# Kernel optimization log

Measured on AMD Instinct MI355X. Metric: run time of the kernel, lower is better.

Reference implementation:

```python
import jax, jax.numpy as jnp
import numpy as np
from jax import lax

DN = ('NCH', 'OIH', 'NCH')

def conv1d(x, w, b, pad=0):
    y = lax.conv_general_dilated(x, w, window_strides=(1,), padding=[(pad, pad)], dimension_numbers=DN)
    return y + b[None, :, None]

def conv_transpose1d(x, w_torch, b):
    # torch ConvTranspose1d weight: [C_in, C_out, K]; equivalent to full conv with flipped kernel
    k = w_torch.shape[-1]
    w = jnp.flip(jnp.transpose(w_torch, (1, 0, 2)), axis=-1)  # [C_out, C_in, K]
    y = lax.conv_general_dilated(x, w, window_strides=(1,), padding=[(k - 1, k - 1)], dimension_numbers=DN)
    return y + b[None, :, None]

def converter(signal, w1, b1, w2, b2, wt, bt, w3, b3):
    h = jax.nn.relu(conv1d(signal, w1, b1))          # [B,10,n-2]
    h = jax.nn.relu(conv1d(h, w2, b2))               # [B,10,n-2]
    h = jax.nn.relu(conv_transpose1d(h, wt, bt))     # [B,10,n]
    h = jax.nn.sigmoid(conv1d(h, w3, b3))            # [B,2,n]
    return h

def setup_inputs() -> dict:
    key = jax.random.key(0)
    ks = jax.random.split(key, 12)
    B, C, n = 32, 128, 8192
    signal = jax.random.normal(ks[0], (B, C, n), dtype=jnp.float32)
    curr_diag = jax.random.uniform(ks[1], (B, n - 1), dtype=jnp.float32) + 0.5
    s = 0.1
    return {
        'signal': signal,
        'curr_diag': curr_diag,
        'index_diag': 1,
        'w1': jax.random.normal(ks[2], (10, C, 3), dtype=jnp.float32) * s,
        'b1': jax.random.normal(ks[3], (10,), dtype=jnp.float32) * s,
        'w2': jax.random.normal(ks[4], (10, 10, 1), dtype=jnp.float32) * s,
        'b2': jax.random.normal(ks[5], (10,), dtype=jnp.float32) * s,
        'wt': jax.random.normal(ks[6], (10, 10, 3), dtype=jnp.float32) * s,
        'bt': jax.random.normal(ks[7], (10,), dtype=jnp.float32) * s,
        'w3': jax.random.normal(ks[8], (2, 10, 1), dtype=jnp.float32) * s,
        'b3': jax.random.normal(ks[9], (2,), dtype=jnp.float32) * s,
        'const': jnp.float32(0.99),
    }

def reference(signal, curr_diag, index_diag, w1, b1, w2, b2, wt, bt, w3, b3, const):
    n = signal.shape[-1]
    lr = converter(signal, w1, b1, w2, b2, wt, bt, w3, b3)  # [B,2,n]
    left, right = lr[:, 0, :], lr[:, 1, :]
    # diag_len = n - index_diag; next diag has length diag_len - 1
    mass_in = curr_diag[:, 1:] * right[:, 1:n - index_diag]
    mass_in = mass_in + curr_diag[:, :-1] * left[:, index_diag:n - 1]
    mass_out = right[:, 0:n - index_diag - 1] + left[:, index_diag + 1:n]
    next_diag = const * mass_in / mass_out
    next_diag = jnp.log(next_diag)
    next_diag = next_diag - jnp.mean(next_diag)
    return next_diag
```

## Files before the change

### kernel.cpp

```cpp
#include <hip/hip_runtime.h>
#include <math.h>

#define B   32
#define CIN 128
#define NN  8192
#define N1  8190
#define CH  10

__global__ __launch_bounds__(256) void k1_conv12(
    const float* __restrict__ sig, const float* __restrict__ w1, const float* __restrict__ b1,
    const float* __restrict__ w2, const float* __restrict__ b2, float* __restrict__ h2out)
{
    const int t = blockIdx.x * 256 + threadIdx.x;
    const int b = blockIdx.y;
    if (t >= N1) return;

    float acc[CH];
#pragma unroll
    for (int o = 0; o < CH; ++o) acc[o] = b1[o];

    const float* sp = sig + (size_t)b * CIN * NN + t;
    for (int ci = 0; ci < CIN; ++ci) {
        const float s0 = sp[(size_t)ci * NN + 0];
        const float s1 = sp[(size_t)ci * NN + 1];
        const float s2 = sp[(size_t)ci * NN + 2];
        const float* wp = w1 + ci * 3;
#pragma unroll
        for (int o = 0; o < CH; ++o) {
            acc[o] = fmaf(wp[o * CIN * 3 + 0], s0, acc[o]);
            acc[o] = fmaf(wp[o * CIN * 3 + 1], s1, acc[o]);
            acc[o] = fmaf(wp[o * CIN * 3 + 2], s2, acc[o]);
        }
    }

    float h1[CH];
#pragma unroll
    for (int o = 0; o < CH; ++o) h1[o] = fmaxf(acc[o], 0.f);

#pragma unroll
    for (int o = 0; o < CH; ++o) {
        float a = b2[o];
#pragma unroll
        for (int i = 0; i < CH; ++i) a = fmaf(w2[o * CH + i], h1[i], a);
        h2out[((size_t)b * CH + o) * N1 + t] = fmaxf(a, 0.f);
    }
}

__global__ __launch_bounds__(256) void k2_convt3(
    const float* __restrict__ h2, const float* __restrict__ wt, const float* __restrict__ bt,
    const float* __restrict__ w3, const float* __restrict__ b3, float* __restrict__ lr)
{
    const int t = blockIdx.x * 256 + threadIdx.x;
    const int b = blockIdx.y;
    if (t >= NN) return;

    float acc[CH];
#pragma unroll
    for (int o = 0; o < CH; ++o) acc[o] = bt[o];

#pragma unroll
    for (int i = 0; i < CH; ++i) {
        const float* hp = h2 + ((size_t)b * CH + i) * N1;
        const float v0 = (t < N1)               ? hp[t]     : 0.f;
        const float v1 = (t >= 1 && t <= N1)    ? hp[t - 1] : 0.f;
        const float v2 = (t >= 2)               ? hp[t - 2] : 0.f;
        const float* wp = wt + (i * CH) * 3;
#pragma unroll
        for (int o = 0; o < CH; ++o) {
            acc[o] = fmaf(wp[o * 3 + 0], v0, acc[o]);
            acc[o] = fmaf(wp[o * 3 + 1], v1, acc[o]);
            acc[o] = fmaf(wp[o * 3 + 2], v2, acc[o]);
        }
    }

    float l = b3[0], r = b3[1];
#pragma unroll
    for (int o = 0; o < CH; ++o) {
        const float h3 = fmaxf(acc[o], 0.f);
        l = fmaf(w3[o],      h3, l);
        r = fmaf(w3[CH + o], h3, r);
    }
    l = 1.f / (1.f + expf(-l));
    r = 1.f / (1.f + expf(-r));

    lr[((size_t)b * 2 + 0) * NN + t] = l;
    lr[((size_t)b * 2 + 1) * NN + t] = r;
}

__global__ __launch_bounds__(256) void k3_diag(
    const float* __restrict__ lr, const float* __restrict__ cd,
    const float* __restrict__ cstp, float* __restrict__ outv, float* __restrict__ bsums)
{
    const int t = blockIdx.x * 256 + threadIdx.x;
    const int b = blockIdx.y;
    float v = 0.f;
    if (t < N1) {
        const float c0 = cd[(size_t)b * (NN - 1) + t];
        const float c1 = cd[(size_t)b * (NN - 1) + t + 1];
        const float* lp = lr + (size_t)b * 2 * NN;
        const float* rp = lp + NN;
        const float mi = c1 * rp[t + 1] + c0 * lp[t + 1];
        const float mo = rp[t] + lp[t + 2];
        v = logf(cstp[0] * mi / mo);
        outv[(size_t)b * N1 + t] = v;
    }
    __shared__ float red[256];
    red[threadIdx.x] = v;
    __syncthreads();
#pragma unroll
    for (int s = 128; s > 0; s >>= 1) {
        if (threadIdx.x < s) red[threadIdx.x] += red[threadIdx.x + s];
        __syncthreads();
    }
    if (threadIdx.x == 0) bsums[blockIdx.y * gridDim.x + blockIdx.x] = red[0];
}

__global__ __launch_bounds__(256) void k4_mean(const float* __restrict__ bsums, float* __restrict__ meanp)
{
    __shared__ float red[256];
    float s = 0.f;
    for (int i = threadIdx.x; i < 1024; i += 256) s += bsums[i];
    red[threadIdx.x] = s;
    __syncthreads();
#pragma unroll
    for (int st = 128; st > 0; st >>= 1) {
        if (threadIdx.x < st) red[threadIdx.x] += red[threadIdx.x + st];
        __syncthreads();
    }
    if (threadIdx.x == 0) meanp[0] = red[0] / (float)(B * N1);
}

__global__ __launch_bounds__(256) void k5_sub(float* __restrict__ outv, const float* __restrict__ meanp, int n)
{
    const int i = blockIdx.x * 256 + threadIdx.x;
    if (i < n) outv[i] -= meanp[0];
}

extern "C" void kernel_launch(void* const* d_in, const int* in_sizes, int n_in,
                              void* d_out, int out_size, void* d_ws, size_t ws_size,
                              hipStream_t stream)
{
    const float* sig = (const float*)d_in[0];
    const float* cd  = (const float*)d_in[1];
    const float* w1  = (const float*)d_in[3];
    const float* b1  = (const float*)d_in[4];
    const float* w2  = (const float*)d_in[5];
    const float* b2  = (const float*)d_in[6];
    const float* wt  = (const float*)d_in[7];
    const float* bt  = (const float*)d_in[8];
    const float* w3  = (const float*)d_in[9];
    const float* b3  = (const float*)d_in[10];
    const float* cst = (const float*)d_in[11];

    float* outv = (float*)d_out;

    float* ws   = (float*)d_ws;
    float* h2   = ws;
    float* lr   = h2 + (size_t)B * CH * N1;
    float* bsum = lr + (size_t)B * 2 * NN;
    float* mean = bsum + 1024;

    dim3 blk(256);
    dim3 g1((N1 + 255) / 256, B);
    dim3 g2(NN / 256, B);

    k1_conv12<<<g1, blk, 0, stream>>>(sig, w1, b1, w2, b2, h2);
    k2_convt3<<<g2, blk, 0, stream>>>(h2, wt, bt, w3, b3, lr);
    k3_diag  <<<g1, blk, 0, stream>>>(lr, cd, cst, outv, bsum);
    k4_mean  <<<dim3(1), blk, 0, stream>>>(bsum, mean);
    k5_sub   <<<dim3((out_size + 255) / 256), blk, 0, stream>>>(outv, mean, out_size);
}
```

Before: 258.5 us.

## Fuse transposed conv with diag kernel and compute two outputs per thread in conv1

The first conv kernel now has each thread compute two adjacent time positions, using float2 loads so the three-tap window overlaps between them and weight loads are shared. The transposed-conv/sigmoid kernel is fused with the diagonal/log kernel, keeping the left/right gates in shared memory with a small halo instead of round-tripping through global memory. This drops one launch and the lr buffer traffic. The cost is a few redundant halo positions per tile, computed by a second pass of the loop, and halving conv1's thread count, which lowers occupancy on a memory-bound kernel.

```diff
diff --git a/kernel.cpp b/kernel.cpp
--- a/kernel.cpp
+++ b/kernel.cpp
@@ -1,109 +1,120 @@
 #include <hip/hip_runtime.h>
 #include <math.h>
 
-#define B   32
-#define CIN 128
-#define NN  8192
-#define N1  8190
-#define CH  10
+#define B    32
+#define CIN  128
+#define NN   8192
+#define N1   8190
+#define CH   10
+#define TILE 256
 
 __global__ __launch_bounds__(256) void k1_conv12(
     const float* __restrict__ sig, const float* __restrict__ w1, const float* __restrict__ b1,
     const float* __restrict__ w2, const float* __restrict__ b2, float* __restrict__ h2out)
 {
-    const int t = blockIdx.x * 256 + threadIdx.x;
-    const int b = blockIdx.y;
-    if (t >= N1) return;
+    const int p  = blockIdx.x * 256 + threadIdx.x;
+    const int t2 = 2 * p;
+    const int b  = blockIdx.y;
+    if (t2 >= N1) return;
 
-    float acc[CH];
+    float y0[CH], y1[CH];
 #pragma unroll
-    for (int o = 0; o < CH; ++o) acc[o] = b1[o];
+    for (int o = 0; o < CH; ++o) { y0[o] = b1[o]; y1[o] = b1[o]; }
 
-    const float* sp = sig + (size_t)b * CIN * NN + t;
+    const float* sp = sig + (size_t)b * CIN * NN + t2;
+
+#pragma unroll 4
     for (int ci = 0; ci < CIN; ++ci) {
-        const float s0 = sp[(size_t)ci * NN + 0];
-        const float s1 = sp[(size_t)ci * NN + 1];
-        const float s2 = sp[(size_t)ci * NN + 2];
+        const float* s = sp + (size_t)ci * NN;
+        const float2 lo = *(const float2*)(s);
+        const float2 hi = *(const float2*)(s + 2);
         const float* wp = w1 + ci * 3;
 #pragma unroll
         for (int o = 0; o < CH; ++o) {
-            acc[o] = fmaf(wp[o * CIN * 3 + 0], s0, acc[o]);
-            acc[o] = fmaf(wp[o * CIN * 3 + 1], s1, acc[o]);
-            acc[o] = fmaf(wp[o * CIN * 3 + 2], s2, acc[o]);
+            const float w0 = wp[o * CIN * 3 + 0];
+            const float w1v = wp[o * CIN * 3 + 1];
+            const float w2v = wp[o * CIN * 3 + 2];
+            y0[o] = fmaf(w0, lo.x, y0[o]);
+            y0[o] = fmaf(w1v, lo.y, y0[o]);
+            y0[o] = fmaf(w2v, hi.x, y0[o]);
+            y1[o] = fmaf(w0, lo.y, y1[o]);
+            y1[o] = fmaf(w1v, hi.x, y1[o]);
+            y1[o] = fmaf(w2v, hi.y, y1[o]);
         }
     }
 
-    float h1[CH];
 #pragma unroll
-    for (int o = 0; o < CH; ++o) h1[o] = fmaxf(acc[o], 0.f);
+    for (int o = 0; o < CH; ++o) { y0[o] = fmaxf(y0[o], 0.f); y1[o] = fmaxf(y1[o], 0.f); }
 
 #pragma unroll
     for (int o = 0; o < CH; ++o) {
-        float a = b2[o];
+        float a0 = b2[o], a1 = b2[o];
 #pragma unroll
-        for (int i = 0; i < CH; ++i) a = fmaf(w2[o * CH + i], h1[i], a);
-        h2out[((size_t)b * CH + o) * N1 + t] = fmaxf(a, 0.f);
+        for (int i = 0; i < CH; ++i) {
+            const float w = w2[o * CH + i];
+            a0 = fmaf(w, y0[i], a0);
+            a1 = fmaf(w, y1[i], a1);
+        }
+        float2 st; st.x = fmaxf(a0, 0.f); st.y = fmaxf(a1, 0.f);
+        *(float2*)(h2out + ((size_t)b * CH + o) * N1 + t2) = st;
     }
 }
 
-__global__ __launch_bounds__(256) void k2_convt3(
-    const float* __restrict__ h2, const float* __restrict__ wt, const float* __restrict__ bt,
-    const float* __restrict__ w3, const float* __restrict__ b3, float* __restrict__ lr)
+__global__ __launch_bounds__(256) void k2_fused(
+    const float* __restrict__ h2, const float* __restrict__ cd,
+    const float* __restrict__ wt, const float* __restrict__ bt,
+    const float* __restrict__ w3, const float* __restrict__ b3,
+    const float* __restrict__ cstp, float* __restrict__ outv, float* __restrict__ bsums)
 {
-    const int t = blockIdx.x * 256 + threadIdx.x;
-    const int b = blockIdx.y;
-    if (t >= NN) return;
+    const int b  = blockIdx.y;
+    const int t0 = blockIdx.x * TILE;
 
-    float acc[CH];
+    __shared__ float lsh[TILE + 4];
+    __shared__ float rsh[TILE + 4];
+
+    for (int s = t0 + threadIdx.x; s <= t0 + TILE + 2; s += 256) {
+        if (s < NN) {
+            float acc[CH];
 #pragma unroll
-    for (int o = 0; o < CH; ++o) acc[o] = bt[o];
-
+            for (int o = 0; o < CH; ++o) acc[o] = bt[o];
 #pragma unroll
-    for (int i = 0; i < CH; ++i) {
-        const float* hp = h2 + ((size_t)b * CH + i) * N1;
-        const float v0 = (t < N1)               ? hp[t]     : 0.f;
-        const float v1 = (t >= 1 && t <= N1)    ? hp[t - 1] : 0.f;
-        const float v2 = (t >= 2)               ? hp[t - 2] : 0.f;
-        const float* wp = wt + (i * CH) * 3;
+            for (int i = 0; i < CH; ++i) {
+                const float* hp = h2 + ((size_t)b * CH + i) * N1;
+                const float v0 = (s < N1)            ? hp[s]     : 0.f;
+                const float v1 = (s >= 1 && s <= N1) ? hp[s - 1] : 0.f;
+                const float v2 = (s >= 2)            ? hp[s - 2] : 0.f;
+                const float* wp = wt + (i * CH) * 3;
 #pragma unroll
-        for (int o = 0; o < CH; ++o) {
-            acc[o] = fmaf(wp[o * 3 + 0], v0, acc[o]);
-            acc[o] = fmaf(wp[o * 3 + 1], v1, acc[o]);
-            acc[o] = fmaf(wp[o * 3 + 2], v2, acc[o]);
+                for (int o = 0; o < CH; ++o) {
+                    acc[o] = fmaf(wp[o * 3 + 0], v0, acc[o]);
+                    acc[o] = fmaf(wp[o * 3 + 1], v1, acc[o]);
+                    acc[o] = fmaf(wp[o * 3 + 2], v2, acc[o]);
+                }
+            }
+            float l = b3[0], r = b3[1];
+#pragma unroll
+            for (int o = 0; o < CH; ++o) {
+                const float h3 = fmaxf(acc[o], 0.f);
+                l = fmaf(w3[o],      h3, l);
+                r = fmaf(w3[CH + o], h3, r);
+            }
+            lsh[s - t0] = 1.f / (1.f + expf(-l));
+            rsh[s - t0] = 1.f / (1.f + expf(-r));
         }
     }
+    __syncthreads();
 
-    float l = b3[0], r = b3[1];
-#pragma unroll
-    for (int o = 0; o < CH; ++o) {
-        const float h3 = fmaxf(acc[o], 0.f);
-        l = fmaf(w3[o],      h3, l);
-        r = fmaf(w3[CH + o], h3, r);
-    }
-    l = 1.f / (1.f + expf(-l));
-    r = 1.f / (1.f + expf(-r));
-
-    lr[((size_t)b * 2 + 0) * NN + t] = l;
-    lr[((size_t)b * 2 + 1) * NN + t] = r;
-}
-
-__global__ __launch_bounds__(256) void k3_diag(
-    const float* __restrict__ lr, const float* __restrict__ cd,
-    const float* __restrict__ cstp, float* __restrict__ outv, float* __restrict__ bsums)
-{
-    const int t = blockIdx.x * 256 + threadIdx.x;
-    const int b = blockIdx.y;
+    const int t = t0 + threadIdx.x;
     float v = 0.f;
     if (t < N1) {
         const float c0 = cd[(size_t)b * (NN - 1) + t];
         const float c1 = cd[(size_t)b * (NN - 1) + t + 1];
-        const float* lp = lr + (size_t)b * 2 * NN;
-        const float* rp = lp + NN;
-        const float mi = c1 * rp[t + 1] + c0 * lp[t + 1];
-        const float mo = rp[t] + lp[t + 2];
+        const float mi = c1 * rsh[threadIdx.x + 1] + c0 * lsh[threadIdx.x + 1];
+        const float mo = rsh[threadIdx.x] + lsh[threadIdx.x + 2];
         v = logf(cstp[0] * mi / mo);
         outv[(size_t)b * N1 + t] = v;
     }
+
     __shared__ float red[256];
     red[threadIdx.x] = v;
     __syncthreads();
@@ -115,7 +126,7 @@
     if (threadIdx.x == 0) bsums[blockIdx.y * gridDim.x + blockIdx.x] = red[0];
 }
 
-__global__ __launch_bounds__(256) void k4_mean(const float* __restrict__ bsums, float* __restrict__ meanp)
+__global__ __launch_bounds__(256) void k3_mean(const float* __restrict__ bsums, float* __restrict__ meanp)
 {
     __shared__ float red[256];
     float s = 0.f;
@@ -130,7 +141,7 @@
     if (threadIdx.x == 0) meanp[0] = red[0] / (float)(B * N1);
 }
 
-__global__ __launch_bounds__(256) void k5_sub(float* __restrict__ outv, const float* __restrict__ meanp, int n)
+__global__ __launch_bounds__(256) void k4_sub(float* __restrict__ outv, const float* __restrict__ meanp, int n)
 {
     const int i = blockIdx.x * 256 + threadIdx.x;
     if (i < n) outv[i] -= meanp[0];
@@ -156,17 +167,15 @@
 
     float* ws   = (float*)d_ws;
     float* h2   = ws;
-    float* lr   = h2 + (size_t)B * CH * N1;
-    float* bsum = lr + (size_t)B * 2 * NN;
+    float* bsum = h2 + (size_t)B * CH * N1;
     float* mean = bsum + 1024;
 
     dim3 blk(256);
-    dim3 g1((N1 + 255) / 256, B);
-    dim3 g2(NN / 256, B);
+    dim3 g1((N1 / 2 + 255) / 256, B);
+    dim3 g2((N1 + TILE - 1) / TILE, B);
 
     k1_conv12<<<g1, blk, 0, stream>>>(sig, w1, b1, w2, b2, h2);
-    k2_convt3<<<g2, blk, 0, stream>>>(h2, wt, bt, w3, b3, lr);
-    k3_diag  <<<g1, blk, 0, stream>>>(lr, cd, cst, outv, bsum);
-    k4_mean  <<<dim3(1), blk, 0, stream>>>(bsum, mean);
-    k5_sub   <<<dim3((out_size + 255) / 256), blk, 0, stream>>>(outv, mean, out_size);
+    k2_fused <<<g2, blk, 0, stream>>>(h2, cd, wt, bt, w3, b3, cst, outv, bsum);
+    k3_mean  <<<dim3(1), blk, 0, stream>>>(bsum, mean);
+    k4_sub   <<<dim3((out_size + 255) / 256), blk, 0, stream>>>(outv, mean, out_size);
 }
```

After: 270.2 us. 1.05x slower.
